# Optimization experiments

Measured on AMD Instinct MI355X. Metric: run time of the kernel, lower is better.

The kernel has to match this reference:

```python
import jax, jax.numpy as jnp
import numpy as np

B, S, D, H, E = 4, 2048, 1024, 2048, 8
TOP_K = 2


def setup_inputs() -> dict:
    key = jax.random.key(0)
    ks = jax.random.split(key, 6)
    s = 0.02
    x = jax.random.normal(ks[0], (B, S, D), dtype=jnp.float32)
    # torch nn.Linear stores weight as [out_features, in_features]
    W1 = jax.random.normal(ks[1], (E, H, D), dtype=jnp.float32) * s  # dim -> hidden
    W2 = jax.random.normal(ks[2], (E, D, H), dtype=jnp.float32) * s  # hidden -> dim
    W3 = jax.random.normal(ks[3], (E, H, D), dtype=jnp.float32) * s  # dim -> hidden
    gate_w = jax.random.normal(ks[4], (E, D), dtype=jnp.float32) * s
    gate_b = jnp.zeros((E,), dtype=jnp.float32)
    return {"x": x, "W1": W1, "W2": W2, "W3": W3, "gate_w": gate_w, "gate_b": gate_b}


def reference(x, W1, W2, W3, gate_w, gate_b):
    b, s, d = x.shape
    xf = x.reshape(-1, d)                                  # [N, D], N = B*S
    logits = xf @ gate_w.T + gate_b                        # [N, E]
    probs = jax.nn.softmax(logits, axis=-1)
    top2_p, top2_i = jax.lax.top_k(probs, TOP_K)           # [N, 2]
    top2_p = top2_p / jnp.sum(top2_p, axis=-1, keepdims=True)
    out = jnp.zeros_like(xf)
    n_experts = W1.shape[0]
    for e in range(n_experts):  # small fixed expert loop
        # combine weight for tokens routed to expert e (0 if not routed)
        coef = jnp.sum(jnp.where(top2_i == e, top2_p, 0.0), axis=-1)  # [N]
        h = jnp.maximum(xf @ W1[e].T, 0.0) ** 2 * (xf @ W3[e].T)      # relu(x)^2 * x  [N, H]
        out = out + coef[:, None] * (h @ W2[e].T)                     # [N, D]
    return out.reshape(b, s, d)
```

## Files before the change

kernel.cpp:

```cpp
#include <hip/hip_runtime.h>
#include <hip/hip_fp16.h>
#include <math.h>

#define N_TOK 8192
#define D_DIM 1024
#define H_DIM 2048
#define N_EXP 8
#define CAPL  8192
#define MT1   18

typedef _Float16 f16x8 __attribute__((ext_vector_type(8)));
typedef float    f32x4 __attribute__((ext_vector_type(4)));

__device__ __forceinline__ void gload16(const void* g, void* l) {
  __builtin_amdgcn_global_load_lds(
      (const __attribute__((address_space(1))) void*)g,
      (__attribute__((address_space(3))) void*)l, 16, 0, 0);
}

__global__ __launch_bounds__(256) void cvt_f32_f16(const float* __restrict__ s,
                                                   _Float16* __restrict__ d, int n4) {
  int i = blockIdx.x * 256 + threadIdx.x;
  if (i >= n4) return;
  float4 v = ((const float4*)s)[i];
  _Float16 o0 = (_Float16)v.x, o1 = (_Float16)v.y, o2 = (_Float16)v.z, o3 = (_Float16)v.w;
  __attribute__((ext_vector_type(4))) _Float16 o = {o0, o1, o2, o3};
  ((__attribute__((ext_vector_type(4))) _Float16*)d)[i] = o;
}

__global__ __launch_bounds__(256) void pack_w(const float* __restrict__ src,
                                              _Float16* __restrict__ dst,
                                              int R, int K) {
  const int e = blockIdx.z, rt = blockIdx.y, kc = blockIdx.x;
  const int t = threadIdx.x;
  const int r = t >> 1, c = (t & 1) * 16;
  const float* s = src + ((long)e * R + (long)rt * 128 + r) * K + kc * 32 + c;
  const float4 v0 = ((const float4*)s)[0];
  const float4 v1 = ((const float4*)s)[1];
  const float4 v2 = ((const float4*)s)[2];
  const float4 v3 = ((const float4*)s)[3];
  f16x8 o0, o1;
  o0[0]=(_Float16)v0.x; o0[1]=(_Float16)v0.y; o0[2]=(_Float16)v0.z; o0[3]=(_Float16)v0.w;
  o0[4]=(_Float16)v1.x; o0[5]=(_Float16)v1.y; o0[6]=(_Float16)v1.z; o0[7]=(_Float16)v1.w;
  o1[0]=(_Float16)v2.x; o1[1]=(_Float16)v2.y; o1[2]=(_Float16)v2.z; o1[3]=(_Float16)v2.w;
  o1[4]=(_Float16)v3.x; o1[5]=(_Float16)v3.y; o1[6]=(_Float16)v3.z; o1[7]=(_Float16)v3.w;
  _Float16* d = dst + (((long)e * (R >> 7) + rt) * (K >> 5) + kc) * 4096 + t * 16;
  ((f16x8*)d)[0] = o0;
  ((f16x8*)d)[1] = o1;
}

__global__ __launch_bounds__(256) void gate_compute(
    const float* __restrict__ x, const float* __restrict__ gw,
    const float* __restrict__ gb, int* __restrict__ e12,
    float2* __restrict__ pp) {
  __shared__ float sgw[N_EXP * D_DIM];
  for (int i = threadIdx.x; i < N_EXP * D_DIM; i += 256) sgw[i] = gw[i];
  __syncthreads();
  const int w = threadIdx.x >> 6, lane = threadIdx.x & 63;
  const int n = blockIdx.x * 4 + w;
  const float* xp = x + (long)n * D_DIM;
  double acc[N_EXP];
  #pragma unroll
  for (int e = 0; e < N_EXP; e++) acc[e] = 0.0;
  for (int i = 0; i < D_DIM / 64; i++) {
    int d = lane + i * 64;
    double xv = (double)xp[d];
    #pragma unroll
    for (int e = 0; e < N_EXP; e++) acc[e] += xv * (double)sgw[e * D_DIM + d];
  }
  #pragma unroll
  for (int e = 0; e < N_EXP; e++)
    for (int off = 32; off >= 1; off >>= 1)
      acc[e] += __shfl_down(acc[e], off);
  if (lane == 0) {
    double lg[N_EXP];
    #pragma unroll
    for (int e = 0; e < N_EXP; e++) lg[e] = acc[e] + (double)gb[e];
    int i1 = 0;
    for (int e = 1; e < N_EXP; e++) if (lg[e] > lg[i1]) i1 = e;
    int i2 = (i1 == 0) ? 1 : 0;
    for (int e = 0; e < N_EXP; e++) { if (e == i1) continue; if (lg[e] > lg[i2]) i2 = e; }
    double p1 = 1.0 / (1.0 + exp(lg[i2] - lg[i1]));
    double p2 = 1.0 - p1;
    e12[n] = i1 | (i2 << 8);
    pp[n] = make_float2((float)p1, (float)p2);
  }
}

__global__ __launch_bounds__(256) void build_lists(
    const int* __restrict__ e12, const float2* __restrict__ pp,
    int* __restrict__ cnt, int* __restrict__ tokL, float* __restrict__ coefL) {
  const int e = blockIdx.x;
  __shared__ int sbase;
  __shared__ int wsum[4];
  const int w = threadIdx.x >> 6, lane = threadIdx.x & 63;
  if (threadIdx.x == 0) sbase = 0;
  __syncthreads();
  for (int c0 = 0; c0 < N_TOK; c0 += 256) {
    const int n = c0 + threadIdx.x;
    const int v = e12[n];
    const float2 pv = pp[n];
    int slot = -1;
    float p = 0.f;
    if ((v & 255) == e)      { slot = 0; p = pv.x; }
    else if ((v >> 8) == e)  { slot = 1; p = pv.y; }
    const unsigned long long m = __ballot(slot >= 0);
    if (lane == 0) wsum[w] = __popcll(m);
    __syncthreads();
    int wbase = sbase;
    #pragma unroll
    for (int i = 0; i < 4; i++) if (i < w) wbase += wsum[i];
    const int total = wsum[0] + wsum[1] + wsum[2] + wsum[3];
    if (slot >= 0) {
      const int pos = wbase + __popcll(m & ((1ull << lane) - 1ull));
      tokL[e * CAPL + pos] = n * 2 + slot;
      coefL[e * CAPL + pos] = p;
    }
    __syncthreads();
    if (threadIdx.x == 0) sbase += total;
  }
  __syncthreads();
  if (threadIdx.x == 0) cnt[e] = sbase;
}

__global__ __launch_bounds__(640, 4) void ffn_stage1(
    const _Float16* __restrict__ xh, const _Float16* __restrict__ w1p,
    const _Float16* __restrict__ w3p, const int* __restrict__ cnt,
    const int* __restrict__ tokL, _Float16* __restrict__ hbuf) {
  const int lin = blockIdx.x;
  const int xcd = lin & 7;
  const int j   = lin >> 3;
  const int mt  = j % MT1;
  const int gi  = j / MT1;
  const int g   = gi * 8 + xcd;
  const int nt  = g & 15;
  const int e   = g >> 4;
  const int m0 = mt * 128;
  const int c = cnt[e];
  if (m0 >= c) return;

  __shared__ _Float16 Xs[3][4096];
  __shared__ _Float16 W1s[3][4096];
  __shared__ _Float16 W3s[3][4096];
  __shared__ int sEnt[128];

  const int t = threadIdx.x;
  if (t < 128) {
    int idx = m0 + t; if (idx >= c) idx = c - 1;
    sEnt[t] = tokL[e * CAPL + idx];
  }
  __syncthreads();

  if (t >= 512) {
    const int pt = t - 512;
    const int swz = ((pt & 3) ^ ((pt >> 3) & 3)) * 8;
    const _Float16* xsrc[4];
    #pragma unroll
    for (int j2 = 0; j2 < 4; j2++)
      xsrc[j2] = xh + (long)(sEnt[(pt >> 2) + 32 * j2] >> 1) * D_DIM + swz;
    const int po = (pt >> 2) * 32 + swz;
    const _Float16* w1t = w1p + (long)(e * 16 + nt) * 32 * 4096 + po;
    const _Float16* w3t = w3p + (long)(e * 16 + nt) * 32 * 4096 + po;
    const int l0 = pt * 8;

    auto stage = [&](int b, int kc) {
      #pragma unroll
      for (int j2 = 0; j2 < 4; j2++)
        gload16(xsrc[j2] + kc * 32, &Xs[b][l0 + j2 * 1024]);
      #pragma unroll
      for (int j2 = 0; j2 < 4; j2++)
        gload16(w1t + (long)kc * 4096 + j2 * 1024, &W1s[b][l0 + j2 * 1024]);
      #pragma unroll
      for (int j2 = 0; j2 < 4; j2++)
        gload16(w3t + (long)kc * 4096 + j2 * 1024, &W3s[b][l0 + j2 * 1024]);
    };

    stage(0, 0); stage(1, 1);
    __asm__ volatile("s_waitcnt vmcnt(12)\n\ts_barrier");
    for (int kc = 0; kc < 32; ++kc) {
      if (kc + 2 < 32) {
        stage((kc + 2) % 3, kc + 2);
        __asm__ volatile("s_waitcnt vmcnt(12)\n\ts_barrier");
      } else {
        __asm__ volatile("s_waitcnt vmcnt(0)\n\ts_barrier");
      }
    }
    return;
  }

  const int w = t >> 6, lane = t & 63;
  const int wm = (w & 1) * 64, wn = (w >> 1) * 32;
  const int q = lane >> 4, lr = lane & 15;
  const int qs = (q ^ ((lr >> 1) & 3)) * 8;

  f32x4 au[4][2], av[4][2];
  const f32x4 zz = {0.f, 0.f, 0.f, 0.f};
  #pragma unroll
  for (int i = 0; i < 4; i++)
    #pragma unroll
    for (int j2 = 0; j2 < 2; j2++) { au[i][j2] = zz; av[i][j2] = zz; }

  __syncthreads();
  for (int kc = 0; kc < 32; ++kc) {
    const int p = kc % 3;
    f16x8 a[4], b1[2], b3[2];
    #pragma unroll
    for (int i = 0; i < 4; i++)
      a[i]  = *(const f16x8*)(&Xs[p][(wm + i * 16 + lr) * 32 + qs]);
    #pragma unroll
    for (int i = 0; i < 2; i++) {
      b1[i] = *(const f16x8*)(&W1s[p][(wn + i * 16 + lr) * 32 + qs]);
      b3[i] = *(const f16x8*)(&W3s[p][(wn + i * 16 + lr) * 32 + qs]);
    }
    #pragma unroll
    for (int mi = 0; mi < 4; mi++)
      #pragma unroll
      for (int ni = 0; ni < 2; ni++) {
        au[mi][ni] = __builtin_amdgcn_mfma_f32_16x16x32_f16(a[mi], b1[ni], au[mi][ni], 0, 0, 0);
        av[mi][ni] = __builtin_amdgcn_mfma_f32_16x16x32_f16(a[mi], b3[ni], av[mi][ni], 0, 0, 0);
      }
    __syncthreads();
  }

  const long tb = ((long)(e * MT1 + mt) * 64 + nt * 4) * 4096;
  #pragma unroll
  for (int mi = 0; mi < 4; mi++) {
    #pragma unroll
    for (int r = 0; r < 4; r++) {
      int ml = wm + mi * 16 + q * 4 + r;
      if (m0 + ml < c) {
        #pragma unroll
        for (int ni = 0; ni < 2; ni++) {
          int colb = wn + ni * 16;
          float u = au[mi][ni][r];
          float rl = u > 0.f ? u : 0.f;
          float hv = rl * rl * av[mi][ni][r];
          hbuf[tb + (long)(colb >> 5) * 4096 + ml * 32 + (colb & 31) + lr] = (_Float16)hv;
        }
      }
    }
  }
}

__global__ __launch_bounds__(384, 3) void ffn_stage2(
    const _Float16* __restrict__ hbuf, const _Float16* __restrict__ w2p,
    const int* __restrict__ cnt, const int* __restrict__ tokL,
    const float* __restrict__ coefL, float* __restrict__ out) {
  const int lin = blockIdx.x;
  const int xcd = lin & 7;
  const int j   = lin >> 3;
  const int mt  = j % MT1;
  const int gi  = j / MT1;
  const int g   = gi * 8 + xcd;
  const int dt  = g & 7;
  const int ezk = g >> 3;
  const int e   = ezk >> 1, ks = ezk & 1;
  const int m0 = mt * 128;
  const int c = cnt[e];
  if (m0 >= c) return;

  __shared__ _Float16 Hs[3][4096];
  __shared__ _Float16 W2s[3][4096];
  __shared__ int sEnt[128];
  __shared__ float sCoef[128];

  const int t = threadIdx.x;
  if (t < 128) {
    int idx = m0 + t; if (idx >= c) idx = c - 1;
    sEnt[t]  = tokL[e * CAPL + idx];
    sCoef[t] = coefL[e * CAPL + idx];
  }
  __syncthreads();

  if (t >= 256) {
    const int pt = t - 256;
    const int swz = ((pt & 3) ^ ((pt >> 3) & 3)) * 8;
    const int po = (pt >> 2) * 32 + swz;
    const _Float16* hA  = hbuf + ((long)(e * MT1 + mt) * 64 + ks * 32) * 4096 + po;
    const _Float16* w2t = w2p  + ((long)(e * 8 + dt) * 64 + ks * 32) * 4096 + po;
    const int l0 = pt * 8;

    auto stage = [&](int b, int kc) {
      #pragma unroll
      for (int j2 = 0; j2 < 4; j2++)
        gload16(hA + (long)kc * 4096 + j2 * 1024, &Hs[b][l0 + j2 * 1024]);
      #pragma unroll
      for (int j2 = 0; j2 < 4; j2++)
        gload16(w2t + (long)kc * 4096 + j2 * 1024, &W2s[b][l0 + j2 * 1024]);
    };

    stage(0, 0); stage(1, 1);
    __asm__ volatile("s_waitcnt vmcnt(8)\n\ts_barrier");
    for (int kc = 0; kc < 32; ++kc) {
      if (kc + 2 < 32) {
        stage((kc + 2) % 3, kc + 2);
        __asm__ volatile("s_waitcnt vmcnt(8)\n\ts_barrier");
      } else {
        __asm__ volatile("s_waitcnt vmcnt(0)\n\ts_barrier");
      }
    }
    return;
  }

  const int w = t >> 6, lane = t & 63;
  const int wm = (w & 1) * 64, wn = (w >> 1) * 64;
  const int q = lane >> 4, lr = lane & 15;
  const int qs = (q ^ ((lr >> 1) & 3)) * 8;

  f32x4 ac[4][4];
  const f32x4 zz = {0.f, 0.f, 0.f, 0.f};
  #pragma unroll
  for (int i = 0; i < 4; i++)
    #pragma unroll
    for (int j2 = 0; j2 < 4; j2++) ac[i][j2] = zz;

  __syncthreads();
  for (int kc = 0; kc < 32; ++kc) {
    const int p = kc % 3;
    f16x8 a[4], b[4];
    #pragma unroll
    for (int i = 0; i < 4; i++) {
      a[i] = *(const f16x8*)(&Hs[p][(wm + i * 16 + lr) * 32 + qs]);
      b[i] = *(const f16x8*)(&W2s[p][(wn + i * 16 + lr) * 32 + qs]);
    }
    #pragma unroll
    for (int mi = 0; mi < 4; mi++)
      #pragma unroll
      for (int ni = 0; ni < 4; ni++)
        ac[mi][ni] = __builtin_amdgcn_mfma_f32_16x16x32_f16(a[mi], b[ni], ac[mi][ni], 0, 0, 0);
    __syncthreads();
  }

  const int n0 = dt * 128;
  #pragma unroll
  for (int mi = 0; mi < 4; mi++) {
    #pragma unroll
    for (int r = 0; r < 4; r++) {
      int ml = wm + mi * 16 + q * 4 + r;
      if (m0 + ml < c) {
        int token = sEnt[ml] >> 1;
        float cf = sCoef[ml];
        float* op = out + (long)token * D_DIM + n0 + wn + lr;
        #pragma unroll
        for (int ni = 0; ni < 4; ni++)
          atomicAdd(op + ni * 16, cf * ac[mi][ni][r]);
      }
    }
  }
}

extern "C" void kernel_launch(void* const* d_in, const int* in_sizes, int n_in,
                              void* d_out, int out_size, void* d_ws, size_t ws_size,
                              hipStream_t stream) {
  (void)in_sizes; (void)n_in; (void)out_size; (void)ws_size;
  const float* x  = (const float*)d_in[0];
  const float* W1 = (const float*)d_in[1];
  const float* W2 = (const float*)d_in[2];
  const float* W3 = (const float*)d_in[3];
  const float* gw = (const float*)d_in[4];
  const float* gb = (const float*)d_in[5];
  float* out = (float*)d_out;

  _Float16* xh  = (_Float16*)d_ws;
  _Float16* w1p = xh  + (size_t)N_TOK * D_DIM;
  _Float16* w3p = w1p + (size_t)N_EXP * H_DIM * D_DIM;
  _Float16* w2p = w3p + (size_t)N_EXP * H_DIM * D_DIM;
  _Float16* hb  = w2p + (size_t)N_EXP * H_DIM * D_DIM;
  int*   cnt   = (int*)(hb + (size_t)N_EXP * MT1 * 64 * 4096);
  int*   tokL  = cnt + 16;
  float* coefL = (float*)(tokL + N_EXP * CAPL);
  int*   e12   = (int*)(coefL + N_EXP * CAPL);
  float2* pp   = (float2*)(e12 + N_TOK);

  hipMemsetAsync(d_out, 0, (size_t)N_TOK * D_DIM * sizeof(float), stream);

  int xn4 = N_TOK * D_DIM / 4;
  cvt_f32_f16<<<(xn4 + 255) / 256, 256, 0, stream>>>(x, xh, xn4);
  pack_w<<<dim3(D_DIM / 32, H_DIM / 128, N_EXP), 256, 0, stream>>>(W1, w1p, H_DIM, D_DIM);
  pack_w<<<dim3(D_DIM / 32, H_DIM / 128, N_EXP), 256, 0, stream>>>(W3, w3p, H_DIM, D_DIM);
  pack_w<<<dim3(H_DIM / 32, D_DIM / 128, N_EXP), 256, 0, stream>>>(W2, w2p, D_DIM, H_DIM);

  gate_compute<<<N_TOK / 4, 256, 0, stream>>>(x, gw, gb, e12, pp);
  build_lists<<<N_EXP, 256, 0, stream>>>(e12, pp, cnt, tokL, coefL);

  ffn_stage1<<<MT1 * 16 * N_EXP, 640, 0, stream>>>(xh, w1p, w3p, cnt, tokL, hb);
  ffn_stage2<<<MT1 * 8 * N_EXP * 2, 384, 0, stream>>>(hb, w2p, cnt, tokL, coefL, out);
}
```

Measured before the change: 622.0 us.

## Replace atomic scatter in stage2 with per-slot fp16 buffer and combine kernel

Stage2 no longer splits K into two halves; each block covers the full hidden dimension and writes coefficient-scaled results as fp16 into a per-expert-slot buffer that reuses the W1 packed workspace. A new combine kernel gathers the two expert rows for each token through an inverse map built in build_lists and writes fp32 output, which removes the output memset and the float atomics. The cost is half as many stage2 blocks with twice the K loop each, an extra pass over an fp16 intermediate, and rounding the partial outputs to fp16.

```diff
diff --git a/kernel.cpp b/kernel.cpp
--- a/kernel.cpp
+++ b/kernel.cpp
@@ -8,6 +8,7 @@
 #define N_EXP 8
 #define CAPL  8192
 #define MT1   18
+#define CAPE  (MT1 * 128)
 
 typedef _Float16 f16x8 __attribute__((ext_vector_type(8)));
 typedef float    f32x4 __attribute__((ext_vector_type(4)));
@@ -89,7 +90,8 @@
 
 __global__ __launch_bounds__(256) void build_lists(
     const int* __restrict__ e12, const float2* __restrict__ pp,
-    int* __restrict__ cnt, int* __restrict__ tokL, float* __restrict__ coefL) {
+    int* __restrict__ cnt, int* __restrict__ tokL, float* __restrict__ coefL,
+    int* __restrict__ inv) {
   const int e = blockIdx.x;
   __shared__ int sbase;
   __shared__ int wsum[4];
@@ -115,6 +117,7 @@
       const int pos = wbase + __popcll(m & ((1ull << lane) - 1ull));
       tokL[e * CAPL + pos] = n * 2 + slot;
       coefL[e * CAPL + pos] = p;
+      inv[n * 2 + slot] = e * CAPE + pos;
     }
     __syncthreads();
     if (threadIdx.x == 0) sbase += total;
@@ -244,8 +247,8 @@
 
 __global__ __launch_bounds__(384, 3) void ffn_stage2(
     const _Float16* __restrict__ hbuf, const _Float16* __restrict__ w2p,
-    const int* __restrict__ cnt, const int* __restrict__ tokL,
-    const float* __restrict__ coefL, float* __restrict__ out) {
+    const int* __restrict__ cnt, const float* __restrict__ coefL,
+    _Float16* __restrict__ obuf) {
   const int lin = blockIdx.x;
   const int xcd = lin & 7;
   const int j   = lin >> 3;
@@ -253,21 +256,18 @@
   const int gi  = j / MT1;
   const int g   = gi * 8 + xcd;
   const int dt  = g & 7;
-  const int ezk = g >> 3;
-  const int e   = ezk >> 1, ks = ezk & 1;
+  const int e   = g >> 3;
   const int m0 = mt * 128;
   const int c = cnt[e];
   if (m0 >= c) return;
 
   __shared__ _Float16 Hs[3][4096];
   __shared__ _Float16 W2s[3][4096];
-  __shared__ int sEnt[128];
   __shared__ float sCoef[128];
 
   const int t = threadIdx.x;
   if (t < 128) {
     int idx = m0 + t; if (idx >= c) idx = c - 1;
-    sEnt[t]  = tokL[e * CAPL + idx];
     sCoef[t] = coefL[e * CAPL + idx];
   }
   __syncthreads();
@@ -276,8 +276,8 @@
     const int pt = t - 256;
     const int swz = ((pt & 3) ^ ((pt >> 3) & 3)) * 8;
     const int po = (pt >> 2) * 32 + swz;
-    const _Float16* hA  = hbuf + ((long)(e * MT1 + mt) * 64 + ks * 32) * 4096 + po;
-    const _Float16* w2t = w2p  + ((long)(e * 8 + dt) * 64 + ks * 32) * 4096 + po;
+    const _Float16* hA  = hbuf + (long)(e * MT1 + mt) * 64 * 4096 + po;
+    const _Float16* w2t = w2p  + (long)(e * 8 + dt) * 64 * 4096 + po;
     const int l0 = pt * 8;
 
     auto stage = [&](int b, int kc) {
@@ -291,8 +291,8 @@
 
     stage(0, 0); stage(1, 1);
     __asm__ volatile("s_waitcnt vmcnt(8)\n\ts_barrier");
-    for (int kc = 0; kc < 32; ++kc) {
-      if (kc + 2 < 32) {
+    for (int kc = 0; kc < 64; ++kc) {
+      if (kc + 2 < 64) {
         stage((kc + 2) % 3, kc + 2);
         __asm__ volatile("s_waitcnt vmcnt(8)\n\ts_barrier");
       } else {
@@ -315,7 +315,7 @@
     for (int j2 = 0; j2 < 4; j2++) ac[i][j2] = zz;
 
   __syncthreads();
-  for (int kc = 0; kc < 32; ++kc) {
+  for (int kc = 0; kc < 64; ++kc) {
     const int p = kc % 3;
     f16x8 a[4], b[4];
     #pragma unroll
@@ -338,14 +338,40 @@
     for (int r = 0; r < 4; r++) {
       int ml = wm + mi * 16 + q * 4 + r;
       if (m0 + ml < c) {
-        int token = sEnt[ml] >> 1;
         float cf = sCoef[ml];
-        float* op = out + (long)token * D_DIM + n0 + wn + lr;
+        _Float16* op = obuf + ((long)(e * CAPE + m0 + ml)) * D_DIM + n0 + wn + lr;
         #pragma unroll
         for (int ni = 0; ni < 4; ni++)
-          atomicAdd(op + ni * 16, cf * ac[mi][ni][r]);
+          op[ni * 16] = (_Float16)(cf * ac[mi][ni][r]);
       }
     }
+  }
+}
+
+__global__ __launch_bounds__(256) void combine_out(
+    const _Float16* __restrict__ obuf, const int* __restrict__ inv,
+    float* __restrict__ out) {
+  const int n = blockIdx.x * 4 + (threadIdx.x >> 6);
+  const int lane = threadIdx.x & 63;
+  const long r1 = (long)inv[n * 2] * D_DIM;
+  const long r2 = (long)inv[n * 2 + 1] * D_DIM;
+  const int c0 = lane * 16;
+  float* op = out + (long)n * D_DIM + c0;
+  #pragma unroll
+  for (int h = 0; h < 2; h++) {
+    f16x8 v1 = *(const f16x8*)(obuf + r1 + c0 + h * 8);
+    f16x8 v2 = *(const f16x8*)(obuf + r2 + c0 + h * 8);
+    float4 o0, o1;
+    o0.x = (float)v1[0] + (float)v2[0];
+    o0.y = (float)v1[1] + (float)v2[1];
+    o0.z = (float)v1[2] + (float)v2[2];
+    o0.w = (float)v1[3] + (float)v2[3];
+    o1.x = (float)v1[4] + (float)v2[4];
+    o1.y = (float)v1[5] + (float)v2[5];
+    o1.z = (float)v1[6] + (float)v2[6];
+    o1.w = (float)v1[7] + (float)v2[7];
+    ((float4*)(op + h * 8))[0] = o0;
+    ((float4*)(op + h * 8))[1] = o1;
   }
 }
 
@@ -371,8 +397,8 @@
   float* coefL = (float*)(tokL + N_EXP * CAPL);
   int*   e12   = (int*)(coefL + N_EXP * CAPL);
   float2* pp   = (float2*)(e12 + N_TOK);
-
-  hipMemsetAsync(d_out, 0, (size_t)N_TOK * D_DIM * sizeof(float), stream);
+  int*   inv   = (int*)(pp + N_TOK);
+  _Float16* obuf = w1p;
 
   int xn4 = N_TOK * D_DIM / 4;
   cvt_f32_f16<<<(xn4 + 255) / 256, 256, 0, stream>>>(x, xh, xn4);
@@ -381,8 +407,9 @@
   pack_w<<<dim3(H_DIM / 32, D_DIM / 128, N_EXP), 256, 0, stream>>>(W2, w2p, D_DIM, H_DIM);
 
   gate_compute<<<N_TOK / 4, 256, 0, stream>>>(x, gw, gb, e12, pp);
-  build_lists<<<N_EXP, 256, 0, stream>>>(e12, pp, cnt, tokL, coefL);
+  build_lists<<<N_EXP, 256, 0, stream>>>(e12, pp, cnt, tokL, coefL, inv);
 
   ffn_stage1<<<MT1 * 16 * N_EXP, 640, 0, stream>>>(xh, w1p, w3p, cnt, tokL, hb);
-  ffn_stage2<<<MT1 * 8 * N_EXP * 2, 384, 0, stream>>>(hb, w2p, cnt, tokL, coefL, out);
-}
+  ffn_stage2<<<MT1 * 8 * N_EXP, 384, 0, stream>>>(hb, w2p, cnt, coefL, obuf);
+  combine_out<<<N_TOK / 4, 256, 0, stream>>>(obuf, inv, out);
+}
```

Result: faster. 582.8 us (-6.3%).
